# Kernel optimization log

Measured on AMD Instinct MI355X. Metric: run time of the kernel, lower is better.

## Reference

```python
import jax, jax.numpy as jnp
import numpy as np

D_MODEL = 1024
D_HEAD = 64


def setup_inputs() -> dict:
    key = jax.random.key(0)
    k_x, k_q, k_k, k_v, k_o = jax.random.split(key, 5)
    scale = 1.0 / np.sqrt(D_MODEL)
    residual_stream = jax.random.normal(k_x, (4, 2048, D_MODEL), dtype=jnp.float32)
    Q = scale * jax.random.normal(k_q, (D_MODEL, D_HEAD), dtype=jnp.float32)
    K = scale * jax.random.normal(k_k, (D_MODEL, D_HEAD), dtype=jnp.float32)
    V = scale * jax.random.normal(k_v, (D_MODEL, D_HEAD), dtype=jnp.float32)
    O = scale * jax.random.normal(k_o, (D_MODEL, D_HEAD), dtype=jnp.float32)
    return {"residual_stream": residual_stream, "Q": Q, "K": K, "V": V, "O": O}


def reference(residual_stream, Q, K, V, O) -> jnp.ndarray:
    # queries/keys: [B, S, d_head]
    queries = jnp.einsum('bsd,dh->bsh', residual_stream, Q)
    keys = jnp.einsum('bsd,dh->bsh', residual_stream, K)
    # NOTE: original module applies NO 1/sqrt(d_head) scaling.
    pre_attention = jnp.einsum('bqh,bkh->bqk', queries, keys)  # [B, S, S]
    S = pre_attention.shape[-1]
    causal = jnp.tril(jnp.ones((S, S), dtype=bool))
    pre_attention = jnp.where(causal[None], pre_attention, -jnp.inf)
    attention = jax.nn.softmax(pre_attention, axis=-1)
    # x = residual @ V @ O^T : [B, S, d_model]
    x = jnp.einsum('bsd,dh,eh->bse', residual_stream, V, O)
    return jnp.einsum('bqk,bke->bqe', attention, x)
```

## Files before the change

### kernel.cpp

```cpp
#include <hip/hip_runtime.h>
#include <hip/hip_bf16.h>
#include <math.h>

#define BATCH 4
#define SEQ   2048
#define DM    1024
#define DH    64
#define NROWS (BATCH*SEQ)

typedef __hip_bfloat16 bf16;
typedef __attribute__((ext_vector_type(8))) short short8;
typedef __attribute__((ext_vector_type(4))) float floatx4;

__device__ __forceinline__ ushort f2bf(float f) {
    union { bf16 h; ushort u; } cv;
    cv.h = __float2bfloat16(f);
    return cv.u;
}
__device__ __forceinline__ float bf2f(ushort u) {
    union { unsigned int i; float f; } v; v.i = ((unsigned int)u) << 16; return v.f;
}

__device__ __forceinline__ void load_lds16(const ushort* g, ushort* l) {
    __builtin_amdgcn_global_load_lds(
        (const __attribute__((address_space(1))) unsigned int*)g,
        (__attribute__((address_space(3))) unsigned int*)l, 16, 0, 0);
}

__global__ __launch_bounds__(256) void wprep_kernel(
    const float* __restrict__ Q, const float* __restrict__ K,
    const float* __restrict__ V, ushort* __restrict__ WhT, ushort* __restrict__ WlT)
{
    int n = blockIdx.x;
    const float* W = (n < 64) ? Q : (n < 128) ? K : V;
    int c = n & 63;
    for (int k = threadIdx.x; k < DM; k += 256) {
        float w = W[k * DH + c];
        ushort hi = f2bf(w);
        WhT[n * DM + k] = hi;
        WlT[n * DM + k] = f2bf(w - bf2f(hi));
    }
}

__global__ __launch_bounds__(256) void qkv_part_kernel(
    const float* __restrict__ x, const ushort* __restrict__ WhT,
    const ushort* __restrict__ WlT, float* __restrict__ Cpart)
{
    __shared__ __align__(16) ushort Xs[2][32][34];
    __shared__ __align__(16) ushort Ws[2][192][34];
    int s0 = blockIdx.x * 32;
    int kb = blockIdx.y * 256;
    int t = threadIdx.x;
    int wave = t >> 6, lane = t & 63, m_ = lane & 15, qd = lane >> 4;
    const floatx4 z4 = {0.f, 0.f, 0.f, 0.f};
    floatx4 accq[2] = {z4, z4}, acck[2] = {z4, z4}, accv[2] = {z4, z4};
    int xr = t >> 3, xc = (t & 7) * 4;
    for (int k0 = 0; k0 < 256; k0 += 32) {
        float4 v = *(const float4*)&x[(size_t)(s0 + xr) * DM + kb + k0 + xc];
        ushort h0 = f2bf(v.x), h1 = f2bf(v.y), h2 = f2bf(v.z), h3 = f2bf(v.w);
        *(ushort4*)&Xs[0][xr][xc] = make_ushort4(h0, h1, h2, h3);
        *(ushort4*)&Xs[1][xr][xc] = make_ushort4(
            f2bf(v.x - bf2f(h0)), f2bf(v.y - bf2f(h1)),
            f2bf(v.z - bf2f(h2)), f2bf(v.w - bf2f(h3)));
        #pragma unroll
        for (int j = 0; j < 3; ++j) {
            int idx = t + j * 256, n = idx >> 2, kc = (idx & 3) * 8;
            *(uint4*)&Ws[0][n][kc] = *(const uint4*)&WhT[n * DM + kb + k0 + kc];
            *(uint4*)&Ws[1][n][kc] = *(const uint4*)&WlT[n * DM + kb + k0 + kc];
        }
        __syncthreads();
        short8 ah[2], al[2];
        #pragma unroll
        for (int mi = 0; mi < 2; ++mi) {
            ah[mi] = *(const short8*)&Xs[0][mi * 16 + m_][qd * 8];
            al[mi] = *(const short8*)&Xs[1][mi * 16 + m_][qd * 8];
        }
        int nq = wave * 16 + m_, nk = 64 + wave * 16 + m_, nv = 128 + wave * 16 + m_;
        short8 bqh = *(const short8*)&Ws[0][nq][qd * 8];
        short8 bql = *(const short8*)&Ws[1][nq][qd * 8];
        short8 bkh = *(const short8*)&Ws[0][nk][qd * 8];
        short8 bkl = *(const short8*)&Ws[1][nk][qd * 8];
        short8 bvh = *(const short8*)&Ws[0][nv][qd * 8];
        #pragma unroll
        for (int mi = 0; mi < 2; ++mi) {
            accq[mi] = __builtin_amdgcn_mfma_f32_16x16x32_bf16(ah[mi], bqh, accq[mi], 0, 0, 0);
            accq[mi] = __builtin_amdgcn_mfma_f32_16x16x32_bf16(al[mi], bqh, accq[mi], 0, 0, 0);
            accq[mi] = __builtin_amdgcn_mfma_f32_16x16x32_bf16(ah[mi], bql, accq[mi], 0, 0, 0);
            acck[mi] = __builtin_amdgcn_mfma_f32_16x16x32_bf16(ah[mi], bkh, acck[mi], 0, 0, 0);
            acck[mi] = __builtin_amdgcn_mfma_f32_16x16x32_bf16(al[mi], bkh, acck[mi], 0, 0, 0);
            acck[mi] = __builtin_amdgcn_mfma_f32_16x16x32_bf16(ah[mi], bkl, acck[mi], 0, 0, 0);
            accv[mi] = __builtin_amdgcn_mfma_f32_16x16x32_bf16(ah[mi], bvh, accv[mi], 0, 0, 0);
        }
        __syncthreads();
    }
    float* Cp = Cpart + (size_t)blockIdx.y * (NROWS * 192);
    #pragma unroll
    for (int mi = 0; mi < 2; ++mi) {
        #pragma unroll
        for (int r = 0; r < 4; ++r) {
            int row = s0 + mi * 16 + qd * 4 + r;
            float* base = Cp + (size_t)row * 192;
            base[wave * 16 + m_]       = accq[mi][r];
            base[64 + wave * 16 + m_]  = acck[mi][r];
            base[128 + wave * 16 + m_] = accv[mi][r];
        }
    }
}

__global__ __launch_bounds__(256) void qkv_reduce_kernel(
    const float* __restrict__ Cpart,
    ushort* __restrict__ qh, ushort* __restrict__ ql,
    ushort* __restrict__ kh, ushort* __restrict__ kl, ushort* __restrict__ xvh)
{
    const size_t SL = (size_t)NROWS * 192;
    int row0 = blockIdx.x * 8;
    int t = threadIdx.x;
    #pragma unroll
    for (int i = 0; i < 6; ++i) {
        int e = i * 256 + t;
        int r = e / 192, c = e - r * 192;
        size_t row = row0 + r;
        size_t off = row * 192 + c;
        float s = Cpart[off] + Cpart[SL + off] + Cpart[2 * SL + off] + Cpart[3 * SL + off];
        ushort hi = f2bf(s);
        ushort lo = f2bf(s - bf2f(hi));
        if (c < 64) {
            qh[row * 64 + c] = hi; ql[row * 64 + c] = lo;
        } else if (c < 128) {
            kh[row * 64 + c - 64] = hi; kl[row * 64 + c - 64] = lo;
        } else {
            xvh[row * 64 + c - 128] = hi;
        }
    }
}

__global__ __launch_bounds__(256) void xvo_kernel(
    const ushort* __restrict__ xvh, const float* __restrict__ O, ushort* __restrict__ xvoT)
{
    __shared__ __align__(16) ushort As[64 * 72];
    __shared__ __align__(16) ushort Bs[64 * 72];
    int e0 = blockIdx.x << 6;
    int row0 = blockIdx.y << 6;
    int t = threadIdx.x;
    int tr = t >> 2, tc = (t & 3) << 4;
    {
        const float* s1 = O + (size_t)(e0 + tr) * DH + tc;
        #pragma unroll
        for (int j = 0; j < 4; ++j) {
            float4 v1 = *(const float4*)(s1 + j * 4);
            uint2 w1;
            w1.x = (uint)f2bf(v1.x) | ((uint)f2bf(v1.y) << 16);
            w1.y = (uint)f2bf(v1.z) | ((uint)f2bf(v1.w) << 16);
            *(uint2*)&As[tr * 72 + tc + j * 4] = w1;
        }
        *(uint4*)&Bs[tr * 72 + tc]     = *(const uint4*)&xvh[(size_t)(row0 + tr) * DH + tc];
        *(uint4*)&Bs[tr * 72 + tc + 8] = *(const uint4*)&xvh[(size_t)(row0 + tr) * DH + tc + 8];
    }
    __syncthreads();
    int wave = t >> 6, lane = t & 63, m_ = lane & 15, qd = lane >> 4;
    const floatx4 z4 = {0.f, 0.f, 0.f, 0.f};
    floatx4 acc[4] = {z4, z4, z4, z4};
    #pragma unroll
    for (int k0 = 0; k0 < 64; k0 += 32) {
        short8 a = *(const short8*)&As[(wave * 16 + m_) * 72 + k0 + qd * 8];
        #pragma unroll
        for (int ni = 0; ni < 4; ++ni) {
            short8 bfr = *(const short8*)&Bs[(ni * 16 + m_) * 72 + k0 + qd * 8];
            acc[ni] = __builtin_amdgcn_mfma_f32_16x16x32_bf16(a, bfr, acc[ni], 0, 0, 0);
        }
    }
    int b = row0 >> 11, sl = row0 & 2047;
    #pragma unroll
    for (int r = 0; r < 4; ++r) {
        int e = e0 + wave * 16 + qd * 4 + r;
        ushort* orow = xvoT + (((size_t)(b * DM + e)) << 11) + sl;
        #pragma unroll
        for (int ni = 0; ni < 4; ++ni)
            orow[ni * 16 + m_] = f2bf(acc[ni][r]);
    }
}

__global__ __launch_bounds__(256) void softmax_kernel(
    const ushort* __restrict__ qh, const ushort* __restrict__ ql,
    const ushort* __restrict__ kh, const ushort* __restrict__ kl,
    ushort* __restrict__ P, float* __restrict__ lpart)
{
    __shared__ __align__(16) ushort Qs[2][2][32][72];
    __shared__ float lred[4][2][32];
    int pp = blockIdx.x & 31, b = blockIdx.x >> 5, s = blockIdx.y;
    int jA = pp, jB = 63 - pp;
    int srowA = jA << 5, srowB = jB << 5;
    int s0gA = (b << 11) + srowA, s0gB = (b << 11) + srowB;
    int t = threadIdx.x, wave = t >> 6, lane = t & 63, m_ = lane & 15, qd = lane >> 4;
    #pragma unroll
    for (int i = 0; i < 4; ++i) {
        int idx = i * 256 + t;
        int tile = idx >> 9, hl = (idx >> 8) & 1, r = (idx >> 3) & 31, c = (idx & 7) * 8;
        const ushort* src = (hl ? ql : qh) + (size_t)((tile ? s0gB : s0gA) + r) * 64 + c;
        *(uint4*)&Qs[tile][hl][r][c] = *(const uint4*)src;
    }
    __syncthreads();
    const ushort* khb = kh + ((size_t)b << 11) * 64;
    const ushort* klb = kl + ((size_t)b << 11) * 64;
    int ntA = (jA >> 1) + 1, ntB = (jB >> 1) + 1;
    int nAs = (ntA > s) ? (((ntA - 1 - s) >> 2) + 1) : 0;
    int nBs = (ntB > s) ? (((ntB - 1 - s) >> 2) + 1) : 0;
    int ntot = nAs + nBs;
    const floatx4 z4 = {0.f, 0.f, 0.f, 0.f};
    float llA[2][4] = {{0.f,0.f,0.f,0.f},{0.f,0.f,0.f,0.f}};
    float llB[2][4] = {{0.f,0.f,0.f,0.f},{0.f,0.f,0.f,0.f}};
    for (int it = wave; it < ntot; it += 4) {
        int isA = (it < nAs);
        int ti = isA ? (s + 4 * it) : (s + 4 * (it - nAs));
        int srow = isA ? srowA : srowB;
        int s0g = isA ? s0gA : s0gB;
        int tidx = isA ? 0 : 1;
        int k0 = ti << 6;
        floatx4 acc[2][4];
        #pragma unroll
        for (int mi = 0; mi < 2; ++mi)
            #pragma unroll
            for (int ni = 0; ni < 4; ++ni) acc[mi][ni] = z4;
        #pragma unroll
        for (int kk = 0; kk < 2; ++kk) {
            short8 ah0 = *(const short8*)&Qs[tidx][0][0 * 16 + m_][kk * 32 + qd * 8];
            short8 ah1 = *(const short8*)&Qs[tidx][0][1 * 16 + m_][kk * 32 + qd * 8];
            short8 al0 = *(const short8*)&Qs[tidx][1][0 * 16 + m_][kk * 32 + qd * 8];
            short8 al1 = *(const short8*)&Qs[tidx][1][1 * 16 + m_][kk * 32 + qd * 8];
            #pragma unroll
            for (int ni = 0; ni < 4; ++ni) {
                size_t koff = (size_t)(k0 + ni * 16 + m_) * 64 + kk * 32 + qd * 8;
                short8 bh = *(const short8*)&khb[koff];
                short8 bl = *(const short8*)&klb[koff];
                acc[0][ni] = __builtin_amdgcn_mfma_f32_16x16x32_bf16(ah0, bh, acc[0][ni], 0, 0, 0);
                acc[0][ni] = __builtin_amdgcn_mfma_f32_16x16x32_bf16(al0, bh, acc[0][ni], 0, 0, 0);
                acc[0][ni] = __builtin_amdgcn_mfma_f32_16x16x32_bf16(ah0, bl, acc[0][ni], 0, 0, 0);
                acc[1][ni] = __builtin_amdgcn_mfma_f32_16x16x32_bf16(ah1, bh, acc[1][ni], 0, 0, 0);
                acc[1][ni] = __builtin_amdgcn_mfma_f32_16x16x32_bf16(al1, bh, acc[1][ni], 0, 0, 0);
                acc[1][ni] = __builtin_amdgcn_mfma_f32_16x16x32_bf16(ah1, bl, acc[1][ni], 0, 0, 0);
            }
        }
        #pragma unroll
        for (int mi = 0; mi < 2; ++mi)
            #pragma unroll
            for (int ni = 0; ni < 4; ++ni) {
                int kc = k0 + ni * 16 + m_;
                #pragma unroll
                for (int r = 0; r < 4; ++r) {
                    int row = srow + mi * 16 + qd * 4 + r;
                    float p = (kc <= row) ? __expf(acc[mi][ni][r]) : 0.f;
                    if (isA) llA[mi][r] += p; else llB[mi][r] += p;
                    P[(size_t)(s0g + mi * 16 + qd * 4 + r) * 2048 + kc] = f2bf(p);
                }
            }
    }
    #pragma unroll
    for (int d = 1; d < 16; d <<= 1)
        #pragma unroll
        for (int mi = 0; mi < 2; ++mi)
            #pragma unroll
            for (int r = 0; r < 4; ++r) {
                llA[mi][r] += __shfl_xor(llA[mi][r], d);
                llB[mi][r] += __shfl_xor(llB[mi][r], d);
            }
    if (m_ == 0)
        #pragma unroll
        for (int mi = 0; mi < 2; ++mi)
            #pragma unroll
            for (int r = 0; r < 4; ++r) {
                lred[wave][0][mi * 16 + qd * 4 + r] = llA[mi][r];
                lred[wave][1][mi * 16 + qd * 4 + r] = llB[mi][r];
            }
    __syncthreads();
    if (t < 64) {
        int tile = t >> 5, row = t & 31;
        float sm = lred[0][tile][row] + lred[1][tile][row]
                 + lred[2][tile][row] + lred[3][tile][row];
        lpart[(size_t)s * NROWS + (tile ? s0gB : s0gA) + row] = sm;
    }
}

__global__ __launch_bounds__(256) void av_kernel(
    const ushort* __restrict__ P, const ushort* __restrict__ xvoT,
    float* __restrict__ out, const float* __restrict__ lpart)
{
    __shared__ __align__(16) ushort AL[2][64 * 64];
    __shared__ __align__(16) ushort AS[2][64 * 64];
    __shared__ __align__(16) ushort Bs[2][128 * 64];
    int bid = blockIdx.x;
    int p = bid >> 5;
    int r5 = bid & 31;
    int b = r5 & 3;
    int n0 = (r5 >> 2) << 7;
    int m0L = (31 - p) << 6, m0S = p << 6;
    int ntk = 32 - p;
    int ntkS = p + 1;
    int t = threadIdx.x, wave = t >> 6, lane = t & 63, m_ = lane & 15, qd = lane >> 4;
    const ushort* Pb = P + ((size_t)b << 22);
    const ushort* Xb = xvoT + ((size_t)(b * DM) << 11);
    const floatx4 z4 = {0.f, 0.f, 0.f, 0.f};
    floatx4 accL[2][4], accS[2][4];
    #pragma unroll
    for (int mi = 0; mi < 2; ++mi)
        #pragma unroll
        for (int ni = 0; ni < 4; ++ni) { accL[mi][ni] = z4; accS[mi][ni] = z4; }
    int mb = (wave >> 1) << 5;
    int nb = (wave & 1) << 6;
    int drow = lane >> 3;
    int dlc = ((lane & 7) ^ drow) << 3;
    #define AV_STAGE(kt, buf)                                                    \
        {                                                                        \
            int k0_ = (kt) << 6;                                                 \
            _Pragma("unroll")                                                    \
            for (int i_ = 0; i_ < 8; ++i_) {                                     \
                int c_ = wave * 8 + i_;                                          \
                if (c_ < 8)                                                      \
                    load_lds16(Pb + (size_t)(m0L + c_ * 8 + drow) * SEQ + k0_ + dlc, \
                               &AL[buf][c_ * 512]);                              \
                else if (c_ < 24)                                                \
                    load_lds16(Xb + (size_t)(n0 + (c_ - 8) * 8 + drow) * SEQ + k0_ + dlc, \
                               &Bs[buf][(c_ - 8) * 512]);                        \
                else if ((kt) < ntkS)                                            \
                    load_lds16(Pb + (size_t)(m0S + (c_ - 24) * 8 + drow) * SEQ + k0_ + dlc, \
                               &AS[buf][(c_ - 24) * 512]);                       \
            }                                                                    \
        }
    AV_STAGE(0, 0)
    for (int kt = 0; kt < ntk; ++kt) {
        __syncthreads();
        if (kt + 1 < ntk) AV_STAGE(kt + 1, (kt + 1) & 1)
        int bufi = kt & 1;
        #pragma unroll
        for (int kk = 0; kk < 2; ++kk) {
            short8 bb[4];
            #pragma unroll
            for (int ni = 0; ni < 4; ++ni) {
                int row = nb + ni * 16 + m_;
                bb[ni] = *(const short8*)&Bs[bufi][row * 64 + (((kk << 2) + qd) ^ (row & 7)) * 8];
            }
            #pragma unroll
            for (int mi = 0; mi < 2; ++mi) {
                int row = mb + mi * 16 + m_;
                short8 aL = *(const short8*)&AL[bufi][row * 64 + (((kk << 2) + qd) ^ (row & 7)) * 8];
                #pragma unroll
                for (int ni = 0; ni < 4; ++ni)
                    accL[mi][ni] = __builtin_amdgcn_mfma_f32_16x16x32_bf16(aL, bb[ni], accL[mi][ni], 0, 0, 0);
            }
            if (kt < ntkS) {
                #pragma unroll
                for (int mi = 0; mi < 2; ++mi) {
                    int row = mb + mi * 16 + m_;
                    short8 aS = *(const short8*)&AS[bufi][row * 64 + (((kk << 2) + qd) ^ (row & 7)) * 8];
                    #pragma unroll
                    for (int ni = 0; ni < 4; ++ni)
                        accS[mi][ni] = __builtin_amdgcn_mfma_f32_16x16x32_bf16(aS, bb[ni], accS[mi][ni], 0, 0, 0);
                }
            }
        }
    }
    float* ob = out + (size_t)b * SEQ * DM;
    #pragma unroll
    for (int mi = 0; mi < 2; ++mi) {
        #pragma unroll
        for (int r = 0; r < 4; ++r) {
            int rowL = m0L + mb + mi * 16 + qd * 4 + r;
            int rowS = m0S + mb + mi * 16 + qd * 4 + r;
            int rgL = (b << 11) + rowL, rgS = (b << 11) + rowS;
            float scL = 1.f / (lpart[rgL] + lpart[NROWS + rgL] + lpart[2*NROWS + rgL] + lpart[3*NROWS + rgL]);
            float scS = 1.f / (lpart[rgS] + lpart[NROWS + rgS] + lpart[2*NROWS + rgS] + lpart[3*NROWS + rgS]);
            float* orL = ob + (size_t)rowL * DM + n0 + nb;
            float* orS = ob + (size_t)rowS * DM + n0 + nb;
            #pragma unroll
            for (int ni = 0; ni < 4; ++ni) {
                orL[ni * 16 + m_] = accL[mi][ni][r] * scL;
                orS[ni * 16 + m_] = accS[mi][ni][r] * scS;
            }
        }
    }
}

extern "C" void kernel_launch(void* const* d_in, const int* in_sizes, int n_in,
                              void* d_out, int out_size, void* d_ws, size_t ws_size,
                              hipStream_t stream) {
    const float* x = (const float*)d_in[0];
    const float* Q = (const float*)d_in[1];
    const float* K = (const float*)d_in[2];
    const float* V = (const float*)d_in[3];
    const float* O = (const float*)d_in[4];
    float* out = (float*)d_out;

    char* ws = (char*)d_ws;
    ushort* qh   = (ushort*)(ws);
    ushort* ql   = (ushort*)(ws + (1ull  << 20));
    ushort* kh   = (ushort*)(ws + (2ull  << 20));
    ushort* kl   = (ushort*)(ws + (3ull  << 20));
    ushort* xvh  = (ushort*)(ws + (4ull  << 20));
    ushort* WhT  = (ushort*)(ws + (5ull  << 20));
    ushort* WlT  = (ushort*)(ws + (5ull  << 20) + (512ull << 10));
    float*  lpart = (float*)(ws + (6ull  << 20));
    ushort* xvoT = (ushort*)(ws + (7ull  << 20));
    ushort* Pbuf = (ushort*)(ws + (23ull << 20));
    float*  Cpart = (float*)(ws + (23ull << 20));

    wprep_kernel<<<192, 256, 0, stream>>>(Q, K, V, WhT, WlT);
    qkv_part_kernel<<<dim3(NROWS / 32, 4), 256, 0, stream>>>(x, WhT, WlT, Cpart);
    qkv_reduce_kernel<<<NROWS / 8, 256, 0, stream>>>(Cpart, qh, ql, kh, kl, xvh);
    xvo_kernel<<<dim3(DM / 64, NROWS / 64), 256, 0, stream>>>(xvh, O, xvoT);
    softmax_kernel<<<dim3(32 * BATCH, 4), 256, 0, stream>>>(qh, ql, kh, kl, Pbuf, lpart);
    av_kernel<<<16 * 8 * 4, 256, 0, stream>>>(Pbuf, xvoT, out, lpart);
}
```

Baseline: 174.1 us.

## Reassociate attention to apply O after PV, split PV over key dimension

Computes P·(xV) in the 64-wide head space and multiplies by O afterwards, instead of first forming the 1024-wide xV·O^T and running the big PV matmul against it. The xvo kernel is removed. qkv_reduce now writes a transposed xV directly. The PV kernel splits the key range eight ways into fp32 partial buffers, and a new out kernel reduces them, normalises by the softmax sum and applies O with split-bf16 MFMAs. This removes roughly 16x of the PV MFMA work and the large xvoT traffic, at the cost of extra partial-sum memory traffic and one more launch.

```diff
diff --git a/kernel.cpp b/kernel.cpp
--- a/kernel.cpp
+++ b/kernel.cpp
@@ -7,9 +7,11 @@
 #define DM    1024
 #define DH    64
 #define NROWS (BATCH*SEQ)
+#define PVSPLIT 8
 
 typedef __hip_bfloat16 bf16;
 typedef __attribute__((ext_vector_type(8))) short short8;
+typedef __attribute__((ext_vector_type(8))) unsigned short ushortx8;
 typedef __attribute__((ext_vector_type(4))) float floatx4;
 
 __device__ __forceinline__ ushort f2bf(float f) {
@@ -110,74 +112,35 @@
 __global__ __launch_bounds__(256) void qkv_reduce_kernel(
     const float* __restrict__ Cpart,
     ushort* __restrict__ qh, ushort* __restrict__ ql,
-    ushort* __restrict__ kh, ushort* __restrict__ kl, ushort* __restrict__ xvh)
-{
+    ushort* __restrict__ kh, ushort* __restrict__ kl, ushort* __restrict__ xvhT)
+{
+    __shared__ ushort xvs[32][72];
     const size_t SL = (size_t)NROWS * 192;
-    int row0 = blockIdx.x * 8;
+    int row0 = blockIdx.x * 32;
     int t = threadIdx.x;
     #pragma unroll
-    for (int i = 0; i < 6; ++i) {
+    for (int i = 0; i < 24; ++i) {
         int e = i * 256 + t;
         int r = e / 192, c = e - r * 192;
         size_t row = row0 + r;
         size_t off = row * 192 + c;
         float s = Cpart[off] + Cpart[SL + off] + Cpart[2 * SL + off] + Cpart[3 * SL + off];
         ushort hi = f2bf(s);
-        ushort lo = f2bf(s - bf2f(hi));
         if (c < 64) {
-            qh[row * 64 + c] = hi; ql[row * 64 + c] = lo;
+            qh[row * 64 + c] = hi; ql[row * 64 + c] = f2bf(s - bf2f(hi));
         } else if (c < 128) {
-            kh[row * 64 + c - 64] = hi; kl[row * 64 + c - 64] = lo;
+            kh[row * 64 + c - 64] = hi; kl[row * 64 + c - 64] = f2bf(s - bf2f(hi));
         } else {
-            xvh[row * 64 + c - 128] = hi;
-        }
-    }
-}
-
-__global__ __launch_bounds__(256) void xvo_kernel(
-    const ushort* __restrict__ xvh, const float* __restrict__ O, ushort* __restrict__ xvoT)
-{
-    __shared__ __align__(16) ushort As[64 * 72];
-    __shared__ __align__(16) ushort Bs[64 * 72];
-    int e0 = blockIdx.x << 6;
-    int row0 = blockIdx.y << 6;
-    int t = threadIdx.x;
-    int tr = t >> 2, tc = (t & 3) << 4;
-    {
-        const float* s1 = O + (size_t)(e0 + tr) * DH + tc;
-        #pragma unroll
-        for (int j = 0; j < 4; ++j) {
-            float4 v1 = *(const float4*)(s1 + j * 4);
-            uint2 w1;
-            w1.x = (uint)f2bf(v1.x) | ((uint)f2bf(v1.y) << 16);
-            w1.y = (uint)f2bf(v1.z) | ((uint)f2bf(v1.w) << 16);
-            *(uint2*)&As[tr * 72 + tc + j * 4] = w1;
-        }
-        *(uint4*)&Bs[tr * 72 + tc]     = *(const uint4*)&xvh[(size_t)(row0 + tr) * DH + tc];
-        *(uint4*)&Bs[tr * 72 + tc + 8] = *(const uint4*)&xvh[(size_t)(row0 + tr) * DH + tc + 8];
+            xvs[r][c - 128] = hi;
+        }
     }
     __syncthreads();
-    int wave = t >> 6, lane = t & 63, m_ = lane & 15, qd = lane >> 4;
-    const floatx4 z4 = {0.f, 0.f, 0.f, 0.f};
-    floatx4 acc[4] = {z4, z4, z4, z4};
-    #pragma unroll
-    for (int k0 = 0; k0 < 64; k0 += 32) {
-        short8 a = *(const short8*)&As[(wave * 16 + m_) * 72 + k0 + qd * 8];
-        #pragma unroll
-        for (int ni = 0; ni < 4; ++ni) {
-            short8 bfr = *(const short8*)&Bs[(ni * 16 + m_) * 72 + k0 + qd * 8];
-            acc[ni] = __builtin_amdgcn_mfma_f32_16x16x32_bf16(a, bfr, acc[ni], 0, 0, 0);
-        }
-    }
+    int h = t >> 2, seg = t & 3;
+    ushortx8 v;
+    #pragma unroll
+    for (int k = 0; k < 8; ++k) v[k] = xvs[seg * 8 + k][h];
     int b = row0 >> 11, sl = row0 & 2047;
-    #pragma unroll
-    for (int r = 0; r < 4; ++r) {
-        int e = e0 + wave * 16 + qd * 4 + r;
-        ushort* orow = xvoT + (((size_t)(b * DM + e)) << 11) + sl;
-        #pragma unroll
-        for (int ni = 0; ni < 4; ++ni)
-            orow[ni * 16 + m_] = f2bf(acc[ni][r]);
-    }
+    *(ushortx8*)&xvhT[(((size_t)(b * 64 + h)) << 11) + sl + seg * 8] = v;
 }
 
 __global__ __launch_bounds__(256) void softmax_kernel(
@@ -280,61 +243,61 @@
     }
 }
 
-__global__ __launch_bounds__(256) void av_kernel(
-    const ushort* __restrict__ P, const ushort* __restrict__ xvoT,
-    float* __restrict__ out, const float* __restrict__ lpart)
+__global__ __launch_bounds__(256) void pv_kernel(
+    const ushort* __restrict__ P, const ushort* __restrict__ xvhT,
+    float* __restrict__ AxvPart)
 {
     __shared__ __align__(16) ushort AL[2][64 * 64];
     __shared__ __align__(16) ushort AS[2][64 * 64];
-    __shared__ __align__(16) ushort Bs[2][128 * 64];
+    __shared__ __align__(16) ushort Bs[2][64 * 64];
     int bid = blockIdx.x;
     int p = bid >> 5;
-    int r5 = bid & 31;
-    int b = r5 & 3;
-    int n0 = (r5 >> 2) << 7;
+    int b = (bid >> 3) & 3;
+    int s = bid & 7;
     int m0L = (31 - p) << 6, m0S = p << 6;
-    int ntk = 32 - p;
-    int ntkS = p + 1;
+    int ntL = 32 - p, ntS = p + 1;
+    int nL = (ntL - s + 7) >> 3;
+    int nS = (ntS > s) ? ((ntS - s + 7) >> 3) : 0;
     int t = threadIdx.x, wave = t >> 6, lane = t & 63, m_ = lane & 15, qd = lane >> 4;
     const ushort* Pb = P + ((size_t)b << 22);
-    const ushort* Xb = xvoT + ((size_t)(b * DM) << 11);
+    const ushort* Xb = xvhT + ((size_t)(b * 64) << 11);
     const floatx4 z4 = {0.f, 0.f, 0.f, 0.f};
-    floatx4 accL[2][4], accS[2][4];
+    floatx4 accL[2][2], accS[2][2];
     #pragma unroll
     for (int mi = 0; mi < 2; ++mi)
         #pragma unroll
-        for (int ni = 0; ni < 4; ++ni) { accL[mi][ni] = z4; accS[mi][ni] = z4; }
+        for (int ni = 0; ni < 2; ++ni) { accL[mi][ni] = z4; accS[mi][ni] = z4; }
     int mb = (wave >> 1) << 5;
-    int nb = (wave & 1) << 6;
+    int nb = (wave & 1) << 5;
     int drow = lane >> 3;
     int dlc = ((lane & 7) ^ drow) << 3;
-    #define AV_STAGE(kt, buf)                                                    \
+    #define PV_STAGE(tt, buf)                                                    \
         {                                                                        \
-            int k0_ = (kt) << 6;                                                 \
+            int k0_ = (s + 8 * (tt)) << 6;                                       \
             _Pragma("unroll")                                                    \
-            for (int i_ = 0; i_ < 8; ++i_) {                                     \
-                int c_ = wave * 8 + i_;                                          \
+            for (int i_ = 0; i_ < 6; ++i_) {                                     \
+                int c_ = wave * 6 + i_;                                          \
                 if (c_ < 8)                                                      \
                     load_lds16(Pb + (size_t)(m0L + c_ * 8 + drow) * SEQ + k0_ + dlc, \
                                &AL[buf][c_ * 512]);                              \
-                else if (c_ < 24)                                                \
-                    load_lds16(Xb + (size_t)(n0 + (c_ - 8) * 8 + drow) * SEQ + k0_ + dlc, \
+                else if (c_ < 16)                                                \
+                    load_lds16(Xb + (size_t)((c_ - 8) * 8 + drow) * SEQ + k0_ + dlc, \
                                &Bs[buf][(c_ - 8) * 512]);                        \
-                else if ((kt) < ntkS)                                            \
-                    load_lds16(Pb + (size_t)(m0S + (c_ - 24) * 8 + drow) * SEQ + k0_ + dlc, \
-                               &AS[buf][(c_ - 24) * 512]);                       \
+                else if ((tt) < nS)                                              \
+                    load_lds16(Pb + (size_t)(m0S + (c_ - 16) * 8 + drow) * SEQ + k0_ + dlc, \
+                               &AS[buf][(c_ - 16) * 512]);                       \
             }                                                                    \
         }
-    AV_STAGE(0, 0)
-    for (int kt = 0; kt < ntk; ++kt) {
+    PV_STAGE(0, 0)
+    for (int tt = 0; tt < nL; ++tt) {
         __syncthreads();
-        if (kt + 1 < ntk) AV_STAGE(kt + 1, (kt + 1) & 1)
-        int bufi = kt & 1;
+        if (tt + 1 < nL) PV_STAGE(tt + 1, (tt + 1) & 1)
+        int bufi = tt & 1;
         #pragma unroll
         for (int kk = 0; kk < 2; ++kk) {
-            short8 bb[4];
-            #pragma unroll
-            for (int ni = 0; ni < 4; ++ni) {
+            short8 bb[2];
+            #pragma unroll
+            for (int ni = 0; ni < 2; ++ni) {
                 int row = nb + ni * 16 + m_;
                 bb[ni] = *(const short8*)&Bs[bufi][row * 64 + (((kk << 2) + qd) ^ (row & 7)) * 8];
             }
@@ -343,39 +306,104 @@
                 int row = mb + mi * 16 + m_;
                 short8 aL = *(const short8*)&AL[bufi][row * 64 + (((kk << 2) + qd) ^ (row & 7)) * 8];
                 #pragma unroll
-                for (int ni = 0; ni < 4; ++ni)
+                for (int ni = 0; ni < 2; ++ni)
                     accL[mi][ni] = __builtin_amdgcn_mfma_f32_16x16x32_bf16(aL, bb[ni], accL[mi][ni], 0, 0, 0);
             }
-            if (kt < ntkS) {
+            if (tt < nS) {
                 #pragma unroll
                 for (int mi = 0; mi < 2; ++mi) {
                     int row = mb + mi * 16 + m_;
                     short8 aS = *(const short8*)&AS[bufi][row * 64 + (((kk << 2) + qd) ^ (row & 7)) * 8];
                     #pragma unroll
-                    for (int ni = 0; ni < 4; ++ni)
+                    for (int ni = 0; ni < 2; ++ni)
                         accS[mi][ni] = __builtin_amdgcn_mfma_f32_16x16x32_bf16(aS, bb[ni], accS[mi][ni], 0, 0, 0);
                 }
             }
         }
     }
-    float* ob = out + (size_t)b * SEQ * DM;
+    float* Ap = AxvPart + (size_t)s * (NROWS * DH);
     #pragma unroll
     for (int mi = 0; mi < 2; ++mi) {
         #pragma unroll
         for (int r = 0; r < 4; ++r) {
             int rowL = m0L + mb + mi * 16 + qd * 4 + r;
             int rowS = m0S + mb + mi * 16 + qd * 4 + r;
-            int rgL = (b << 11) + rowL, rgS = (b << 11) + rowS;
-            float scL = 1.f / (lpart[rgL] + lpart[NROWS + rgL] + lpart[2*NROWS + rgL] + lpart[3*NROWS + rgL]);
-            float scS = 1.f / (lpart[rgS] + lpart[NROWS + rgS] + lpart[2*NROWS + rgS] + lpart[3*NROWS + rgS]);
-            float* orL = ob + (size_t)rowL * DM + n0 + nb;
-            float* orS = ob + (size_t)rowS * DM + n0 + nb;
-            #pragma unroll
-            for (int ni = 0; ni < 4; ++ni) {
-                orL[ni * 16 + m_] = accL[mi][ni][r] * scL;
-                orS[ni * 16 + m_] = accS[mi][ni][r] * scS;
-            }
-        }
+            float* orL = Ap + (size_t)((b << 11) + rowL) * DH + nb;
+            float* orS = Ap + (size_t)((b << 11) + rowS) * DH + nb;
+            #pragma unroll
+            for (int ni = 0; ni < 2; ++ni) {
+                orL[ni * 16 + m_] = accL[mi][ni][r];
+                orS[ni * 16 + m_] = accS[mi][ni][r];
+            }
+        }
+    }
+    #undef PV_STAGE
+}
+
+__global__ __launch_bounds__(256) void out_kernel(
+    const float* __restrict__ AxvPart, const float* __restrict__ lpart,
+    const float* __restrict__ O, float* __restrict__ out)
+{
+    __shared__ __align__(16) ushort As[2][64][72];
+    __shared__ __align__(16) ushort Bsh[2][128][72];
+    __shared__ float lsc[64];
+    int bid = blockIdx.x;
+    int r0 = (bid >> 3) << 6;
+    int e0 = (bid & 7) << 7;
+    int t = threadIdx.x;
+    if (t < 64) {
+        int rg = r0 + t;
+        lsc[t] = 1.f / (lpart[rg] + lpart[NROWS + rg]
+                      + lpart[2 * NROWS + rg] + lpart[3 * NROWS + rg]);
+    }
+    __syncthreads();
+    const size_t PSL = (size_t)NROWS * DH;
+    #pragma unroll
+    for (int i = 0; i < 16; ++i) {
+        int idx = i * 256 + t;
+        int r = idx >> 6, h = idx & 63;
+        size_t off = (size_t)(r0 + r) * DH + h;
+        float a = 0.f;
+        #pragma unroll
+        for (int sp = 0; sp < PVSPLIT; ++sp) a += AxvPart[sp * PSL + off];
+        a *= lsc[r];
+        ushort hi = f2bf(a);
+        As[0][r][h] = hi;
+        As[1][r][h] = f2bf(a - bf2f(hi));
+    }
+    #pragma unroll
+    for (int i = 0; i < 32; ++i) {
+        int idx = i * 256 + t;
+        int r = idx >> 6, h = idx & 63;
+        float w = O[(size_t)(e0 + r) * DH + h];
+        ushort hi = f2bf(w);
+        Bsh[0][r][h] = hi;
+        Bsh[1][r][h] = f2bf(w - bf2f(hi));
+    }
+    __syncthreads();
+    int wave = t >> 6, lane = t & 63, m_ = lane & 15, qd = lane >> 4;
+    const floatx4 z4 = {0.f, 0.f, 0.f, 0.f};
+    floatx4 acc[8] = {z4, z4, z4, z4, z4, z4, z4, z4};
+    #pragma unroll
+    for (int kk = 0; kk < 2; ++kk) {
+        short8 ah = *(const short8*)&As[0][wave * 16 + m_][kk * 32 + qd * 8];
+        short8 al = *(const short8*)&As[1][wave * 16 + m_][kk * 32 + qd * 8];
+        #pragma unroll
+        for (int ni = 0; ni < 8; ++ni) {
+            short8 bh = *(const short8*)&Bsh[0][ni * 16 + m_][kk * 32 + qd * 8];
+            short8 bl = *(const short8*)&Bsh[1][ni * 16 + m_][kk * 32 + qd * 8];
+            acc[ni] = __builtin_amdgcn_mfma_f32_16x16x32_bf16(ah, bh, acc[ni], 0, 0, 0);
+            acc[ni] = __builtin_amdgcn_mfma_f32_16x16x32_bf16(al, bh, acc[ni], 0, 0, 0);
+            acc[ni] = __builtin_amdgcn_mfma_f32_16x16x32_bf16(ah, bl, acc[ni], 0, 0, 0);
+        }
+    }
+    #pragma unroll
+    for (int r = 0; r < 4; ++r) {
+        int row = r0 + wave * 16 + qd * 4 + r;
+        float* orow = out + (size_t)row * DM + e0;
+        #pragma unroll
+        for (int ni = 0; ni < 8; ++ni)
+            orow[ni * 16 + m_] = acc[ni][r];
     }
 }
 
@@ -394,18 +422,18 @@
     ushort* ql   = (ushort*)(ws + (1ull  << 20));
     ushort* kh   = (ushort*)(ws + (2ull  << 20));
     ushort* kl   = (ushort*)(ws + (3ull  << 20));
-    ushort* xvh  = (ushort*)(ws + (4ull  << 20));
+    ushort* xvhT = (ushort*)(ws + (4ull  << 20));
     ushort* WhT  = (ushort*)(ws + (5ull  << 20));
     ushort* WlT  = (ushort*)(ws + (5ull  << 20) + (512ull << 10));
     float*  lpart = (float*)(ws + (6ull  << 20));
-    ushort* xvoT = (ushort*)(ws + (7ull  << 20));
+    float*  AxvPart = (float*)(ws + (7ull << 20));
     ushort* Pbuf = (ushort*)(ws + (23ull << 20));
     float*  Cpart = (float*)(ws + (23ull << 20));
 
     wprep_kernel<<<192, 256, 0, stream>>>(Q, K, V, WhT, WlT);
     qkv_part_kernel<<<dim3(NROWS / 32, 4), 256, 0, stream>>>(x, WhT, WlT, Cpart);
-    qkv_reduce_kernel<<<NROWS / 8, 256, 0, stream>>>(Cpart, qh, ql, kh, kl, xvh);
-    xvo_kernel<<<dim3(DM / 64, NROWS / 64), 256, 0, stream>>>(xvh, O, xvoT);
+    qkv_reduce_kernel<<<NROWS / 32, 256, 0, stream>>>(Cpart, qh, ql, kh, kl, xvhT);
     softmax_kernel<<<dim3(32 * BATCH, 4), 256, 0, stream>>>(qh, ql, kh, kl, Pbuf, lpart);
-    av_kernel<<<16 * 8 * 4, 256, 0, stream>>>(Pbuf, xvoT, out, lpart);
-}
+    pv_kernel<<<16 * 4 * PVSPLIT, 256, 0, stream>>>(Pbuf, xvhT, AxvPart);
+    out_kernel<<<(NROWS / 64) * 8, 256, 0, stream>>>(AxvPart, lpart, O, out);
+}
```

New measurement: 181.6 us. 4.3% more time.
